# Performance work log

Measured on AMD Instinct MI355X. Metric: run time of the kernel, lower is better.

Reference implementation:

```python
import jax, jax.numpy as jnp
import numpy as np

ALPHA = 0.2       # LeakyReLU negative slope
LN_EPS = 1e-5     # nn.LayerNorm default eps
MASK_VAL = -1e9   # masked_fill value in original


def setup_inputs() -> dict:
    key = jax.random.key(0)
    ks = jax.random.split(key, 8)
    B, N, D_IN, D_OUT = 1, 1024, 64, 64
    def lin(k, fan_in, shape):
        return jax.random.normal(k, shape, dtype=jnp.float32) / np.sqrt(fan_in)
    return {
        "h": jax.random.normal(ks[0], (B, N, D_IN), dtype=jnp.float32),
        "adj": jax.random.randint(ks[1], (B, N, N), 0, 2, dtype=jnp.int32),
        "W": lin(ks[2], D_IN, (D_IN, D_OUT)),                 # W (no bias)
        "attn_w1": lin(ks[3], 3 * D_OUT, (3 * D_OUT, D_OUT)),  # attention_mlp layer 1
        "attn_b1": jnp.zeros((D_OUT,), jnp.float32),
        "attn_w2": lin(ks[4], D_OUT, (D_OUT, 1)),              # attention_mlp layer 2
        "attn_b2": jnp.zeros((1,), jnp.float32),
        "edge_w": lin(ks[5], 2 * D_IN, (2 * D_IN, D_OUT)),     # edge_encoder linear
        "edge_b": jnp.zeros((D_OUT,), jnp.float32),
        "ln_g": jnp.ones((D_OUT,), jnp.float32),
        "ln_b": jnp.zeros((D_OUT,), jnp.float32),
    }


def reference(h, adj, W, attn_w1, attn_b1, attn_w2, attn_b2, edge_w, edge_b, ln_g, ln_b):
    # Eval mode: dropout is identity. in_features == out_features -> residual_proj is None.
    d_in = h.shape[-1]
    d = W.shape[1]
    Wh = h @ W  # [b, n, d]

    # Split concat-linears into per-block matmuls (math identical to cat+Linear,
    # avoids materializing the [b,n,n,3d] and [b,n,n,2d] concat tensors).
    E_i, E_j = edge_w[:d_in], edge_w[d_in:]
    ei = h @ E_i  # [b, n, d]
    ej = h @ E_j
    # edge_encoder(cat(h_i, h_j)) -> [b, n, n, d]
    edge = jax.nn.leaky_relu(ei[:, :, None, :] + ej[:, None, :, :] + edge_b, ALPHA)

    A_i, A_j, A_e = attn_w1[:d], attn_w1[d:2 * d], attn_w1[2 * d:]
    pre = ((Wh @ A_i)[:, :, None, :] + (Wh @ A_j)[:, None, :, :]
           + edge @ A_e + attn_b1)                      # [b, n, n, d]
    hid = jax.nn.leaky_relu(pre, ALPHA)
    e = jnp.squeeze(hid @ attn_w2, -1) + attn_b2[0]     # [b, n, n]

    e = jnp.where(adj == 0, MASK_VAL, e)
    attention = jax.nn.softmax(e, axis=-1)              # [b, n, n]

    h_prime = attention @ Wh + h                        # residual (in == out)

    mu = jnp.mean(h_prime, axis=-1, keepdims=True)
    var = jnp.mean(jnp.square(h_prime - mu), axis=-1, keepdims=True)
    out = (h_prime - mu) / jnp.sqrt(var + LN_EPS) * ln_g + ln_b
    return out
```

## Files before the change

kernel.cpp:

```cpp
#include <hip/hip_runtime.h>
#include <math.h>

#define N 1024
#define D 64
#define ALPHA 0.2f
#define LN_EPS 1e-5f
#define MASK_VAL -1000000000.0f

typedef __attribute__((ext_vector_type(8))) short bf16x8;
typedef __attribute__((ext_vector_type(4))) float f32x4;

__device__ __forceinline__ float leaky(float x) { return fmaxf(x, ALPHA * x); }

__device__ __forceinline__ unsigned f2bf_u(float f) {
    unsigned u = __builtin_bit_cast(unsigned, f);
    u += 0x7fffu + ((u >> 16) & 1u);
    return u >> 16;
}
__device__ __forceinline__ short f2bf(float f) { return (short)f2bf_u(f); }

__device__ __forceinline__ unsigned lpk(float x, float y) {
    float lx = fmaxf(x, ALPHA * x);
    float ly = fmaxf(y, ALPHA * y);
    return f2bf_u(lx) | (f2bf_u(ly) << 16);
}

union BF8 { bf16x8 v; unsigned u[4]; };

__global__ __launch_bounds__(256) void gat_precompute(
    const float* __restrict__ h, const float* __restrict__ W,
    const float* __restrict__ attn_w1, const float* __restrict__ attn_b1,
    const float* __restrict__ edge_w, const float* __restrict__ edge_b,
    float* __restrict__ Wh, float* __restrict__ ejB, float* __restrict__ aj,
    float* __restrict__ ei, float* __restrict__ aiB)
{
    const int tid = threadIdx.x;
    const int r = tid >> 6;
    const int k = tid & 63;
    const int i = blockIdx.x * 4 + r;
    __shared__ float hrow[4][D];
    __shared__ float whrow[4][D];

    hrow[r][k] = h[(size_t)i * D + k];
    __syncthreads();

    float wh = 0.f, vei = 0.f, vej = 0.f;
    #pragma unroll 8
    for (int m = 0; m < D; ++m) {
        float hm = hrow[r][m];
        wh  = fmaf(hm, W[m * D + k], wh);
        vei = fmaf(hm, edge_w[m * D + k], vei);
        vej = fmaf(hm, edge_w[(m + D) * D + k], vej);
    }
    Wh[(size_t)i * D + k]  = wh;
    ei[(size_t)i * D + k]  = vei;
    ejB[(size_t)i * D + k] = vej + edge_b[k];
    whrow[r][k] = wh;
    __syncthreads();

    float vai = 0.f, vaj = 0.f;
    #pragma unroll 8
    for (int m = 0; m < D; ++m) {
        float wm = whrow[r][m];
        vai = fmaf(wm, attn_w1[m * D + k], vai);
        vaj = fmaf(wm, attn_w1[(m + D) * D + k], vaj);
    }
    aiB[(size_t)i * D + k] = vai + attn_b1[k];
    aj[(size_t)i * D + k]  = vaj;
}

__global__ __launch_bounds__(256) void gat_scores(
    const float* __restrict__ ejB, const float* __restrict__ aj,
    const float* __restrict__ ei, const float* __restrict__ aiB,
    const float* __restrict__ attn_w1, const float* __restrict__ attn_w2,
    const float* __restrict__ attn_b2, float* __restrict__ e_out)
{
    const int tid  = threadIdx.x;
    const int lane = tid & 63;
    const int wid  = tid >> 6;
    const int nloc = lane & 15;
    const int quad = lane >> 4;
    const int i0   = (blockIdx.x >> 2) * 4;
    const int jb   = (blockIdx.x & 3) * 256 + wid * 64;
    const float* __restrict__ Ae = attn_w1 + 128 * D;

    __shared__ __align__(16) float sv[4][D];
    __shared__ float av[4][D];

    sv[tid >> 6][tid & 63] = ei[(size_t)(i0 + (tid >> 6)) * D + (tid & 63)];
    av[tid >> 6][tid & 63] = aiB[(size_t)(i0 + (tid >> 6)) * D + (tid & 63)];
    __syncthreads();

    bf16x8 Bf[2][4];
    #pragma unroll
    for (int kt = 0; kt < 2; ++kt)
        #pragma unroll
        for (int ot = 0; ot < 4; ++ot)
            #pragma unroll
            for (int idx = 0; idx < 8; ++idx) {
                int k = kt * 32 + quad * 8 + idx;
                Bf[kt][ot][idx] = f2bf(Ae[(size_t)k * D + ot * 16 + nloc]);
            }

    float w2l[4];
    #pragma unroll
    for (int ot = 0; ot < 4; ++ot) w2l[ot] = attn_w2[ot * 16 + nloc];
    const float b2 = attn_b2[0];

    for (int jt = 0; jt < 4; ++jt) {
        const int j16 = jb + jt * 16;
        const float* __restrict__ ejr = ejB + (size_t)(j16 + nloc) * D;

        const int k0 = quad * 8;
        float4 ev0 = *(const float4*)(ejr + k0);
        float4 ev1 = *(const float4*)(ejr + k0 + 4);
        float4 ev2 = *(const float4*)(ejr + 32 + k0);
        float4 ev3 = *(const float4*)(ejr + 32 + k0 + 4);

        f32x4 ajreg[4];
        #pragma unroll
        for (int ot = 0; ot < 4; ++ot)
            #pragma unroll
            for (int r = 0; r < 4; ++r)
                ajreg[ot][r] = aj[(size_t)(j16 + quad * 4 + r) * D + ot * 16 + nloc];

        #pragma unroll
        for (int ii = 0; ii < 4; ++ii) {
            const float4 s0 = *(const float4*)(&sv[ii][k0]);
            const float4 s1 = *(const float4*)(&sv[ii][k0 + 4]);
            const float4 s2 = *(const float4*)(&sv[ii][32 + k0]);
            const float4 s3 = *(const float4*)(&sv[ii][32 + k0 + 4]);

            BF8 af0, af1;
            af0.u[0] = lpk(ev0.x + s0.x, ev0.y + s0.y);
            af0.u[1] = lpk(ev0.z + s0.z, ev0.w + s0.w);
            af0.u[2] = lpk(ev1.x + s1.x, ev1.y + s1.y);
            af0.u[3] = lpk(ev1.z + s1.z, ev1.w + s1.w);
            af1.u[0] = lpk(ev2.x + s2.x, ev2.y + s2.y);
            af1.u[1] = lpk(ev2.z + s2.z, ev2.w + s2.w);
            af1.u[2] = lpk(ev3.x + s3.x, ev3.y + s3.y);
            af1.u[3] = lpk(ev3.z + s3.z, ev3.w + s3.w);

            f32x4 acc[4];
            #pragma unroll
            for (int ot = 0; ot < 4; ++ot) {
                acc[ot] = __builtin_amdgcn_mfma_f32_16x16x32_bf16(af0.v, Bf[0][ot], ajreg[ot], 0, 0, 0);
                acc[ot] = __builtin_amdgcn_mfma_f32_16x16x32_bf16(af1.v, Bf[1][ot], acc[ot], 0, 0, 0);
            }

            float part[4] = {0.f, 0.f, 0.f, 0.f};
            #pragma unroll
            for (int ot = 0; ot < 4; ++ot) {
                const float avli = av[ii][ot * 16 + nloc];
                #pragma unroll
                for (int r = 0; r < 4; ++r) {
                    float pre = acc[ot][r] + avli;
                    part[r] = fmaf(leaky(pre), w2l[ot], part[r]);
                }
            }
            #pragma unroll
            for (int r = 0; r < 4; ++r) {
                float v = part[r];
                v += __shfl_xor(v, 1, 64);
                v += __shfl_xor(v, 2, 64);
                v += __shfl_xor(v, 4, 64);
                v += __shfl_xor(v, 8, 64);
                part[r] = v;
            }
            if (nloc == 0) {
                const int jr = j16 + quad * 4;
                #pragma unroll
                for (int r = 0; r < 4; ++r)
                    e_out[(size_t)(i0 + ii) * N + jr + r] = part[r] + b2;
            }
        }
    }
}

__global__ __launch_bounds__(256) void gat_softagg(
    const float* __restrict__ e_in, const int* __restrict__ adj,
    const float* __restrict__ Wh, const float* __restrict__ h,
    const float* __restrict__ ln_g, const float* __restrict__ ln_b,
    float* __restrict__ out)
{
    const int tid  = threadIdx.x;
    const int lane = tid & 63;
    const int wid  = tid >> 6;
    const int i0   = blockIdx.x * 4;
    const int i    = i0 + wid;

    __shared__ float p[4][N];
    __shared__ float invs[4];
    __shared__ float red[4][4][D];

    {
        const float* __restrict__ erow = e_in + (size_t)i * N;
        const int*   __restrict__ arow = adj  + (size_t)i * N;
        float m = -INFINITY;
        #pragma unroll 4
        for (int c = 0; c < N / 64; ++c) {
            int j = c * 64 + lane;
            float v = erow[j];
            if (arow[j] == 0) v = MASK_VAL;
            p[wid][j] = v;
            m = fmaxf(m, v);
        }
        #pragma unroll
        for (int off = 32; off >= 1; off >>= 1) m = fmaxf(m, __shfl_xor(m, off, 64));
        float s = 0.f;
        #pragma unroll 4
        for (int c = 0; c < N / 64; ++c) {
            int j = c * 64 + lane;
            float pv = __expf(p[wid][j] - m);
            p[wid][j] = pv;
            s += pv;
        }
        #pragma unroll
        for (int off = 32; off >= 1; off >>= 1) s += __shfl_xor(s, off, 64);
        if (lane == 0) invs[wid] = 1.f / s;
    }
    __syncthreads();

    {
        const int k = tid & 63, g = tid >> 6;
        float hp0 = 0.f, hp1 = 0.f, hp2 = 0.f, hp3 = 0.f;
        #pragma unroll 4
        for (int jj = 0; jj < 256; ++jj) {
            const int j = g * 256 + jj;
            const float whv = Wh[(size_t)j * D + k];
            hp0 = fmaf(p[0][j], whv, hp0);
            hp1 = fmaf(p[1][j], whv, hp1);
            hp2 = fmaf(p[2][j], whv, hp2);
            hp3 = fmaf(p[3][j], whv, hp3);
        }
        red[g][0][k] = hp0;
        red[g][1][k] = hp1;
        red[g][2][k] = hp2;
        red[g][3][k] = hp3;
    }
    __syncthreads();

    {
        float v = (red[0][wid][lane] + red[1][wid][lane] +
                   red[2][wid][lane] + red[3][wid][lane]) * invs[wid]
                  + h[(size_t)i * D + lane];
        float mu = v;
        #pragma unroll
        for (int off = 32; off >= 1; off >>= 1) mu += __shfl_xor(mu, off, 64);
        mu *= (1.f / D);
        float d = v - mu;
        float var = d * d;
        #pragma unroll
        for (int off = 32; off >= 1; off >>= 1) var += __shfl_xor(var, off, 64);
        var *= (1.f / D);
        out[(size_t)i * D + lane] = d * rsqrtf(var + LN_EPS) * ln_g[lane] + ln_b[lane];
    }
}

extern "C" void kernel_launch(void* const* d_in, const int* in_sizes, int n_in,
                              void* d_out, int out_size, void* d_ws, size_t ws_size,
                              hipStream_t stream) {
    const float* h       = (const float*)d_in[0];
    const int*   adj     = (const int*)  d_in[1];
    const float* W       = (const float*)d_in[2];
    const float* attn_w1 = (const float*)d_in[3];
    const float* attn_b1 = (const float*)d_in[4];
    const float* attn_w2 = (const float*)d_in[5];
    const float* attn_b2 = (const float*)d_in[6];
    const float* edge_w  = (const float*)d_in[7];
    const float* edge_b  = (const float*)d_in[8];
    const float* ln_g    = (const float*)d_in[9];
    const float* ln_b    = (const float*)d_in[10];
    float* out = (float*)d_out;

    float* ws  = (float*)d_ws;
    float* Wh  = ws + 0 * (N * D);
    float* ejB = ws + 1 * (N * D);
    float* aj  = ws + 2 * (N * D);
    float* ei  = ws + 3 * (N * D);
    float* aiB = ws + 4 * (N * D);
    float* e   = ws + 5 * (N * D);

    gat_precompute<<<N / 4, 256, 0, stream>>>(h, W, attn_w1, attn_b1, edge_w, edge_b,
                                              Wh, ejB, aj, ei, aiB);
    gat_scores<<<(N / 4) * 4, 256, 0, stream>>>(ejB, aj, ei, aiB,
                                                attn_w1, attn_w2, attn_b2, e);
    gat_softagg<<<N / 4, 256, 0, stream>>>(e, adj, Wh, h, ln_g, ln_b, out);
}
```

Before: 138.6 us.

## Transpose MFMA operands, fold adjacency mask into scores, halve softagg rows per block

The scores kernel swaps the MFMA operand order so each lane holds the output features of a single j. This lets the second attention layer be reduced with vector FMAs and two cross-quad shuffles instead of four 16-lane shuffle trees per row. The aiB bias is folded into the accumulator init, bf16 packing uses a byte-permute, and the adjacency mask is applied when writing the scores. The softmax/aggregation kernel no longer reads adj, and it now handles two rows per block with two waves per row, doubling the block count. The trade-off is an extra block barrier and cross-wave max/sum combine, plus less reuse of Wh per load in the aggregation loop.

```diff
diff --git a/kernel.cpp b/kernel.cpp
--- a/kernel.cpp
+++ b/kernel.cpp
@@ -9,8 +9,7 @@
 
 typedef __attribute__((ext_vector_type(8))) short bf16x8;
 typedef __attribute__((ext_vector_type(4))) float f32x4;
-
-__device__ __forceinline__ float leaky(float x) { return fmaxf(x, ALPHA * x); }
+typedef __attribute__((ext_vector_type(2))) float f32x2;
 
 __device__ __forceinline__ unsigned f2bf_u(float f) {
     unsigned u = __builtin_bit_cast(unsigned, f);
@@ -19,10 +18,16 @@
 }
 __device__ __forceinline__ short f2bf(float f) { return (short)f2bf_u(f); }
 
-__device__ __forceinline__ unsigned lpk(float x, float y) {
-    float lx = fmaxf(x, ALPHA * x);
-    float ly = fmaxf(y, ALPHA * y);
-    return f2bf_u(lx) | (f2bf_u(ly) << 16);
+__device__ __forceinline__ unsigned rne_pair(float x, float y) {
+    unsigned ux = __builtin_bit_cast(unsigned, x);
+    unsigned uy = __builtin_bit_cast(unsigned, y);
+    ux += 0x7fffu + ((ux >> 16) & 1u);
+    uy += 0x7fffu + ((uy >> 16) & 1u);
+    return __builtin_amdgcn_perm(uy, ux, 0x07060302);
+}
+
+__device__ __forceinline__ f32x4 leaky4(f32x4 v) {
+    return __builtin_elementwise_max(v, v * 0.2f);
 }
 
 union BF8 { bf16x8 v; unsigned u[4]; };
@@ -73,7 +78,8 @@
     const float* __restrict__ ejB, const float* __restrict__ aj,
     const float* __restrict__ ei, const float* __restrict__ aiB,
     const float* __restrict__ attn_w1, const float* __restrict__ attn_w2,
-    const float* __restrict__ attn_b2, float* __restrict__ e_out)
+    const float* __restrict__ attn_b2, const int* __restrict__ adj,
+    float* __restrict__ e_out)
 {
     const int tid  = threadIdx.x;
     const int lane = tid & 63;
@@ -85,7 +91,7 @@
     const float* __restrict__ Ae = attn_w1 + 128 * D;
 
     __shared__ __align__(16) float sv[4][D];
-    __shared__ float av[4][D];
+    __shared__ __align__(16) float av[4][D];
 
     sv[tid >> 6][tid & 63] = ei[(size_t)(i0 + (tid >> 6)) * D + (tid & 63)];
     av[tid >> 6][tid & 63] = aiB[(size_t)(i0 + (tid >> 6)) * D + (tid & 63)];
@@ -102,148 +108,139 @@
                 Bf[kt][ot][idx] = f2bf(Ae[(size_t)k * D + ot * 16 + nloc]);
             }
 
-    float w2l[4];
+    f32x4 w2l[4];
     #pragma unroll
-    for (int ot = 0; ot < 4; ++ot) w2l[ot] = attn_w2[ot * 16 + nloc];
+    for (int ot = 0; ot < 4; ++ot)
+        w2l[ot] = *(const f32x4*)(attn_w2 + ot * 16 + quad * 4);
     const float b2 = attn_b2[0];
+    const int k0 = quad * 8;
 
     for (int jt = 0; jt < 4; ++jt) {
         const int j16 = jb + jt * 16;
-        const float* __restrict__ ejr = ejB + (size_t)(j16 + nloc) * D;
-
-        const int k0 = quad * 8;
-        float4 ev0 = *(const float4*)(ejr + k0);
-        float4 ev1 = *(const float4*)(ejr + k0 + 4);
-        float4 ev2 = *(const float4*)(ejr + 32 + k0);
-        float4 ev3 = *(const float4*)(ejr + 32 + k0 + 4);
-
-        f32x4 ajreg[4];
+        const int jrow = j16 + nloc;
+        const float* __restrict__ ejr = ejB + (size_t)jrow * D;
+        const float* __restrict__ ajr = aj + (size_t)jrow * D;
+
+        f32x4 ev0 = *(const f32x4*)(ejr + k0);
+        f32x4 ev1 = *(const f32x4*)(ejr + k0 + 4);
+        f32x4 ev2 = *(const f32x4*)(ejr + 32 + k0);
+        f32x4 ev3 = *(const f32x4*)(ejr + 32 + k0 + 4);
+        f32x4 ajv[4];
         #pragma unroll
         for (int ot = 0; ot < 4; ++ot)
-            #pragma unroll
-            for (int r = 0; r < 4; ++r)
-                ajreg[ot][r] = aj[(size_t)(j16 + quad * 4 + r) * D + ot * 16 + nloc];
+            ajv[ot] = *(const f32x4*)(ajr + ot * 16 + quad * 4);
 
         #pragma unroll
         for (int ii = 0; ii < 4; ++ii) {
-            const float4 s0 = *(const float4*)(&sv[ii][k0]);
-            const float4 s1 = *(const float4*)(&sv[ii][k0 + 4]);
-            const float4 s2 = *(const float4*)(&sv[ii][32 + k0]);
-            const float4 s3 = *(const float4*)(&sv[ii][32 + k0 + 4]);
+            const f32x4 s0 = *(const f32x4*)(&sv[ii][k0]);
+            const f32x4 s1 = *(const f32x4*)(&sv[ii][k0 + 4]);
+            const f32x4 s2 = *(const f32x4*)(&sv[ii][32 + k0]);
+            const f32x4 s3 = *(const f32x4*)(&sv[ii][32 + k0 + 4]);
 
             BF8 af0, af1;
-            af0.u[0] = lpk(ev0.x + s0.x, ev0.y + s0.y);
-            af0.u[1] = lpk(ev0.z + s0.z, ev0.w + s0.w);
-            af0.u[2] = lpk(ev1.x + s1.x, ev1.y + s1.y);
-            af0.u[3] = lpk(ev1.z + s1.z, ev1.w + s1.w);
-            af1.u[0] = lpk(ev2.x + s2.x, ev2.y + s2.y);
-            af1.u[1] = lpk(ev2.z + s2.z, ev2.w + s2.w);
-            af1.u[2] = lpk(ev3.x + s3.x, ev3.y + s3.y);
-            af1.u[3] = lpk(ev3.z + s3.z, ev3.w + s3.w);
+            f32x4 t;
+            t = leaky4(ev0 + s0); af0.u[0] = rne_pair(t.x, t.y); af0.u[1] = rne_pair(t.z, t.w);
+            t = leaky4(ev1 + s1); af0.u[2] = rne_pair(t.x, t.y); af0.u[3] = rne_pair(t.z, t.w);
+            t = leaky4(ev2 + s2); af1.u[0] = rne_pair(t.x, t.y); af1.u[1] = rne_pair(t.z, t.w);
+            t = leaky4(ev3 + s3); af1.u[2] = rne_pair(t.x, t.y); af1.u[3] = rne_pair(t.z, t.w);
 
             f32x4 acc[4];
             #pragma unroll
             for (int ot = 0; ot < 4; ++ot) {
-                acc[ot] = __builtin_amdgcn_mfma_f32_16x16x32_bf16(af0.v, Bf[0][ot], ajreg[ot], 0, 0, 0);
-                acc[ot] = __builtin_amdgcn_mfma_f32_16x16x32_bf16(af1.v, Bf[1][ot], acc[ot], 0, 0, 0);
-            }
-
-            float part[4] = {0.f, 0.f, 0.f, 0.f};
+                f32x4 avl = *(const f32x4*)(&av[ii][ot * 16 + quad * 4]);
+                acc[ot] = __builtin_amdgcn_mfma_f32_16x16x32_bf16(Bf[0][ot], af0.v, ajv[ot] + avl, 0, 0, 0);
+                acc[ot] = __builtin_amdgcn_mfma_f32_16x16x32_bf16(Bf[1][ot], af1.v, acc[ot], 0, 0, 0);
+            }
+
+            f32x2 e2 = {0.f, 0.f};
             #pragma unroll
             for (int ot = 0; ot < 4; ++ot) {
-                const float avli = av[ii][ot * 16 + nloc];
-                #pragma unroll
-                for (int r = 0; r < 4; ++r) {
-                    float pre = acc[ot][r] + avli;
-                    part[r] = fmaf(leaky(pre), w2l[ot], part[r]);
-                }
-            }
-            #pragma unroll
-            for (int r = 0; r < 4; ++r) {
-                float v = part[r];
-                v += __shfl_xor(v, 1, 64);
-                v += __shfl_xor(v, 2, 64);
-                v += __shfl_xor(v, 4, 64);
-                v += __shfl_xor(v, 8, 64);
-                part[r] = v;
-            }
-            if (nloc == 0) {
-                const int jr = j16 + quad * 4;
-                #pragma unroll
-                for (int r = 0; r < 4; ++r)
-                    e_out[(size_t)(i0 + ii) * N + jr + r] = part[r] + b2;
+                f32x4 hd = leaky4(acc[ot]);
+                e2 += hd.lo * w2l[ot].lo;
+                e2 += hd.hi * w2l[ot].hi;
+            }
+            float e = e2.x + e2.y;
+            e += __shfl_xor(e, 16, 64);
+            e += __shfl_xor(e, 32, 64);
+
+            if (lane < 16) {
+                const int j = j16 + lane;
+                const size_t idx = (size_t)(i0 + ii) * N + j;
+                const int a = adj[idx];
+                e_out[idx] = a ? (e + b2) : MASK_VAL;
             }
         }
     }
 }
 
 __global__ __launch_bounds__(256) void gat_softagg(
-    const float* __restrict__ e_in, const int* __restrict__ adj,
-    const float* __restrict__ Wh, const float* __restrict__ h,
-    const float* __restrict__ ln_g, const float* __restrict__ ln_b,
-    float* __restrict__ out)
+    const float* __restrict__ e_in, const float* __restrict__ Wh,
+    const float* __restrict__ h, const float* __restrict__ ln_g,
+    const float* __restrict__ ln_b, float* __restrict__ out)
 {
     const int tid  = threadIdx.x;
     const int lane = tid & 63;
     const int wid  = tid >> 6;
-    const int i0   = blockIdx.x * 4;
-    const int i    = i0 + wid;
-
-    __shared__ float p[4][N];
-    __shared__ float invs[4];
-    __shared__ float red[4][4][D];
+    const int i0   = blockIdx.x * 2;
+    const int r    = wid >> 1;
+    const int half = wid & 1;
+
+    __shared__ float p[2][N];
+    __shared__ float wred[4][2];
+    __shared__ float red[4][2][D];
 
     {
-        const float* __restrict__ erow = e_in + (size_t)i * N;
-        const int*   __restrict__ arow = adj  + (size_t)i * N;
+        const float* __restrict__ erow = e_in + (size_t)(i0 + r) * N;
         float m = -INFINITY;
-        #pragma unroll 4
-        for (int c = 0; c < N / 64; ++c) {
-            int j = c * 64 + lane;
+        #pragma unroll
+        for (int c = 0; c < 8; ++c) {
+            int j = half * 512 + c * 64 + lane;
             float v = erow[j];
-            if (arow[j] == 0) v = MASK_VAL;
-            p[wid][j] = v;
+            p[r][j] = v;
             m = fmaxf(m, v);
         }
         #pragma unroll
         for (int off = 32; off >= 1; off >>= 1) m = fmaxf(m, __shfl_xor(m, off, 64));
+        if (lane == 0) wred[wid][0] = m;
+    }
+    __syncthreads();
+    {
+        float m = fmaxf(wred[r * 2][0], wred[r * 2 + 1][0]);
         float s = 0.f;
-        #pragma unroll 4
-        for (int c = 0; c < N / 64; ++c) {
-            int j = c * 64 + lane;
-            float pv = __expf(p[wid][j] - m);
-            p[wid][j] = pv;
+        #pragma unroll
+        for (int c = 0; c < 8; ++c) {
+            int j = half * 512 + c * 64 + lane;
+            float pv = __expf(p[r][j] - m);
+            p[r][j] = pv;
             s += pv;
         }
         #pragma unroll
         for (int off = 32; off >= 1; off >>= 1) s += __shfl_xor(s, off, 64);
-        if (lane == 0) invs[wid] = 1.f / s;
+        if (lane == 0) wred[wid][1] = s;
     }
     __syncthreads();
 
     {
-        const int k = tid & 63, g = tid >> 6;
-        float hp0 = 0.f, hp1 = 0.f, hp2 = 0.f, hp3 = 0.f;
-        #pragma unroll 4
+        const int k = lane, g = wid;
+        float hp0 = 0.f, hp1 = 0.f;
+        #pragma unroll 8
         for (int jj = 0; jj < 256; ++jj) {
             const int j = g * 256 + jj;
             const float whv = Wh[(size_t)j * D + k];
             hp0 = fmaf(p[0][j], whv, hp0);
             hp1 = fmaf(p[1][j], whv, hp1);
-            hp2 = fmaf(p[2][j], whv, hp2);
-            hp3 = fmaf(p[3][j], whv, hp3);
         }
         red[g][0][k] = hp0;
         red[g][1][k] = hp1;
-        red[g][2][k] = hp2;
-        red[g][3][k] = hp3;
-    }
-    __syncthreads();
-
-    {
-        float v = (red[0][wid][lane] + red[1][wid][lane] +
-                   red[2][wid][lane] + red[3][wid][lane]) * invs[wid]
-                  + h[(size_t)i * D + lane];
+    }
+    __syncthreads();
+
+    if (wid < 2) {
+        const int rr = wid;
+        const float inv_s = 1.f / (wred[rr * 2][1] + wred[rr * 2 + 1][1]);
+        float v = (red[0][rr][lane] + red[1][rr][lane] +
+                   red[2][rr][lane] + red[3][rr][lane]) * inv_s
+                  + h[(size_t)(i0 + rr) * D + lane];
         float mu = v;
         #pragma unroll
         for (int off = 32; off >= 1; off >>= 1) mu += __shfl_xor(mu, off, 64);
@@ -253,7 +250,7 @@
         #pragma unroll
         for (int off = 32; off >= 1; off >>= 1) var += __shfl_xor(var, off, 64);
         var *= (1.f / D);
-        out[(size_t)i * D + lane] = d * rsqrtf(var + LN_EPS) * ln_g[lane] + ln_b[lane];
+        out[(size_t)(i0 + rr) * D + lane] = d * rsqrtf(var + LN_EPS) * ln_g[lane] + ln_b[lane];
     }
 }
 
@@ -284,6 +281,6 @@
     gat_precompute<<<N / 4, 256, 0, stream>>>(h, W, attn_w1, attn_b1, edge_w, edge_b,
                                               Wh, ejB, aj, ei, aiB);
     gat_scores<<<(N / 4) * 4, 256, 0, stream>>>(ejB, aj, ei, aiB,
-                                                attn_w1, attn_w2, attn_b2, e);
-    gat_softagg<<<N / 4, 256, 0, stream>>>(e, adj, Wh, h, ln_g, ln_b, out);
-}
+                                                attn_w1, attn_w2, attn_b2, adj, e);
+    gat_softagg<<<N / 2, 256, 0, stream>>>(e, Wh, h, ln_g, ln_b, out);
+}
```

Result: slower. 149.5 us (+7.9%).
